# Kernel tuning notes

Hardware: AMD Instinct MI355X
Metric: run time of the kernel (lower is better)

Reference implementation:

```python
import jax, jax.numpy as jnp
import numpy as np

BITS = 4
PACK = 32 // BITS  # 8 nibbles per int32
GROUPSIZE = 128
MASK = (1 << BITS) - 1


def dequantize(qweight, qzeros, scales):
    """GPTQ dequant: W[i,o] = scales[g[i],o] * (q[i,o] - (z[g[i],o] + 1))."""
    shifts = (jnp.arange(PACK, dtype=jnp.int32) * BITS)
    # qweight: [in/8, out] packed along input dim -> [in, out]
    wq = (qweight[:, None, :] >> shifts[None, :, None]) & MASK
    wq = wq.reshape(-1, qweight.shape[1])  # [in, out] int32 in [0,15]
    # qzeros: [G, out/8] packed along output dim -> [G, out]
    zq = ((qzeros[:, :, None] >> shifts[None, None, :]) & MASK) + 1
    zq = zq.reshape(qzeros.shape[0], -1)  # [G, out]
    g_idx = jnp.arange(wq.shape[0], dtype=jnp.int32) // GROUPSIZE  # [in]
    # fp16 dequant like the CUDA/Triton GPTQ kernels
    W = (wq - zq[g_idx]).astype(jnp.float16) * scales[g_idx]
    return W  # [in, out] fp16


def setup_inputs() -> dict:
    key = jax.random.key(0)
    kx, kw, kz, ks, kb = jax.random.split(key, 5)
    in_f, out_f, groups = 4096, 4096, 4096 // GROUPSIZE
    x = jax.random.normal(kx, (8192, in_f), dtype=jnp.float16)
    qweight = jax.random.randint(kw, (in_f // PACK, out_f), 0, 2147483647, dtype=jnp.int32)
    qzeros = jax.random.randint(kz, (groups, out_f // PACK), 0, 2147483647, dtype=jnp.int32)
    scales = (jax.random.uniform(ks, (groups, out_f), dtype=jnp.float32) * 0.01 + 0.001).astype(jnp.float16)
    bias = jax.random.normal(kb, (out_f,), dtype=jnp.float16)
    return {"x": x, "qweight": qweight, "qzeros": qzeros, "scales": scales, "bias": bias}


def reference(x, qweight, qzeros, scales, bias):
    W = dequantize(qweight, qzeros, scales)  # [in, out] fp16
    # accumulate in fp32, output fp16 (matches CaiGPTQLinearOp fp16 output)
    out = jnp.matmul(x, W, preferred_element_type=jnp.float32).astype(jnp.float16)
    out = out + bias
    return out
```

## Files before the change

kernel.cpp:

```cpp
#include <hip/hip_runtime.h>

typedef _Float16 half8 __attribute__((ext_vector_type(8)));
typedef _Float16 half2v __attribute__((ext_vector_type(2)));
typedef float floatx4 __attribute__((ext_vector_type(4)));

#define K_IN 4096
#define N_OUT 4096
#define NGROUPS 32
#define BM 128
#define BN 128

__device__ __forceinline__ unsigned int pkcvt(float lo, float hi) {
    return __builtin_bit_cast(unsigned int, __builtin_amdgcn_cvt_pkrtz(lo, hi));
}

__device__ __forceinline__ void gll16(const _Float16* g, _Float16* l) {
    __builtin_amdgcn_global_load_lds(
        (const __attribute__((address_space(1))) void*)g,
        (__attribute__((address_space(3))) void*)l, 16, 0, 0);
}

__global__ __launch_bounds__(256)
void cvt_x_f16(const float* __restrict__ x, _Float16* __restrict__ x16) {
    const size_t idx = ((size_t)blockIdx.x * 256 + threadIdx.x) * 8;
    const float4 a = *(const float4*)(x + idx);
    const float4 b = *(const float4*)(x + idx + 4);
    uint4 u;
    u.x = pkcvt(a.x, a.y);  u.y = pkcvt(a.z, a.w);
    u.z = pkcvt(b.x, b.y);  u.w = pkcvt(b.z, b.w);
    *(uint4*)(x16 + idx) = u;
}

__global__ __launch_bounds__(256)
void dequant_wt(const int* __restrict__ qweight,
                const int* __restrict__ qzeros,
                const float* __restrict__ scales,
                _Float16* __restrict__ wt)
{
    const int tid = threadIdx.x;
    const int col = blockIdx.x * 64 + (tid & 63);
    const int g   = blockIdx.y;
    const int i   = tid >> 6;

    const unsigned int zw = (unsigned int)qzeros[g * (N_OUT / 8) + (col >> 3)];
    const unsigned int z  = (zw >> ((col & 7) * 4)) & 0xFu;
    const unsigned int cb = 0x6400u + z + 1u;
    const half2v c2 = __builtin_bit_cast(half2v, cb | (cb << 16));
    const float  s  = scales[g * N_OUT + col];
    const half2v s2 = __builtin_bit_cast(half2v, pkcvt(s, s));

    const int kc0 = g * 16 + i * 4;
#pragma unroll
    for (int r = 0; r < 4; ++r) {
        const unsigned int q = (unsigned int)qweight[(size_t)(kc0 + r) * N_OUT + col];
        const unsigned int r0 = (q & 0x000F000Fu)         | 0x64006400u;
        const unsigned int r1 = ((q >> 4) & 0x000F000Fu)  | 0x64006400u;
        const unsigned int r2 = ((q >> 8) & 0x000F000Fu)  | 0x64006400u;
        const unsigned int r3 = ((q >> 12) & 0x000F000Fu) | 0x64006400u;
        unsigned int p0 = __builtin_bit_cast(unsigned int,
                          (half2v)((__builtin_bit_cast(half2v, r0) - c2) * s2));
        unsigned int p1 = __builtin_bit_cast(unsigned int,
                          (half2v)((__builtin_bit_cast(half2v, r1) - c2) * s2));
        unsigned int p2 = __builtin_bit_cast(unsigned int,
                          (half2v)((__builtin_bit_cast(half2v, r2) - c2) * s2));
        unsigned int p3 = __builtin_bit_cast(unsigned int,
                          (half2v)((__builtin_bit_cast(half2v, r3) - c2) * s2));
        uint4 nat;
        nat.x = (p0 & 0xFFFFu) | (p1 << 16);
        nat.y = (p2 & 0xFFFFu) | (p3 << 16);
        nat.z = (p0 >> 16) | (p1 & 0xFFFF0000u);
        nat.w = (p2 >> 16) | (p3 & 0xFFFF0000u);
        *(uint4*)(wt + (size_t)col * K_IN + (kc0 + r) * 8) = nat;
    }
}

__global__ __launch_bounds__(256, 3)
void gemm_f16(const _Float16* __restrict__ x16,
              const _Float16* __restrict__ wt,
              const float* __restrict__ bias,
              float* __restrict__ out)
{
    __shared__ alignas(16) _Float16 As[2 * BM * 32];

    const int tid  = threadIdx.x;
    const int lane = tid & 63;
    const int wave = tid >> 6;
    const int l15  = lane & 15;
    const int l4   = lane >> 4;

    const int blockN = blockIdx.x * BN;
    const int blockM = blockIdx.y * BM;

    floatx4 acc[8][2] = {};

    const int grow  = wave * 32 + (lane >> 2);
    const int gchnk = (lane & 3) ^ ((lane >> 3) & 3);
    const _Float16* gsrc0 = x16 + (size_t)(blockM + grow) * K_IN + gchnk * 8;
    const _Float16* gsrc1 = gsrc0 + (size_t)16 * K_IN;
    _Float16* ldst0 = &As[wave * 1024];
    _Float16* ldst1 = ldst0 + 512;

    const int rdoff = (l4 ^ ((l15 >> 1) & 3)) * 8;

    int ncol[2];
    const _Float16* wp0;
    const _Float16* wp1;
    ncol[0] = blockN + wave * 32 + l15;
    ncol[1] = ncol[0] + 16;
    wp0 = wt + (size_t)ncol[0] * K_IN + l4 * 8;
    wp1 = wt + (size_t)ncol[1] * K_IN + l4 * 8;

    gll16(gsrc0, ldst0);
    gll16(gsrc1, ldst1);
    __builtin_amdgcn_sched_barrier(0);
    uint4 pw0 = *(const uint4*)(const void*)wp0;
    uint4 pw1 = *(const uint4*)(const void*)wp1;

    for (int t = 0; t < 4 * NGROUPS; ++t) {
        const int buf = t & 1;

        asm volatile("s_waitcnt vmcnt(2)" ::: "memory");
        __builtin_amdgcn_s_barrier();
        asm volatile("" ::: "memory");

        half8 afrag[8];
#pragma unroll
        for (int i = 0; i < 8; ++i)
            afrag[i] = *(const half8*)(const void*)
                &As[buf * 4096 + (i * 16 + l15) * 32 + rdoff];

        half8 b0 = __builtin_bit_cast(half8, pw0);
        half8 b1 = __builtin_bit_cast(half8, pw1);

        const int t1 = (t + 1 < 4 * NGROUPS) ? t + 1 : t;
        const int bn = buf ^ 1;
        gll16(gsrc0 + t1 * 32, ldst0 + bn * 4096);
        gll16(gsrc1 + t1 * 32, ldst1 + bn * 4096);
        __builtin_amdgcn_sched_barrier(0);
        pw0 = *(const uint4*)(const void*)(wp0 + t1 * 32);
        pw1 = *(const uint4*)(const void*)(wp1 + t1 * 32);

#pragma unroll
        for (int i = 0; i < 8; ++i) {
            acc[i][0] = __builtin_amdgcn_mfma_f32_16x16x32_f16(
                afrag[i], b0, acc[i][0], 0, 0, 0);
            acc[i][1] = __builtin_amdgcn_mfma_f32_16x16x32_f16(
                afrag[i], b1, acc[i][1], 0, 0, 0);
        }
    }

#pragma unroll
    for (int j = 0; j < 2; ++j) {
        const int n = ncol[j];
        const float bv = bias[n];
#pragma unroll
        for (int i = 0; i < 8; ++i) {
            const int m = blockM + i * 16 + l4 * 4;
#pragma unroll
            for (int r = 0; r < 4; ++r)
                out[(size_t)(m + r) * N_OUT + n] = acc[i][j][r] + bv;
        }
    }
}

__global__ __launch_bounds__(256, 2)
void gptq_gemm_fused(const float* __restrict__ x,
                     const int*   __restrict__ qweight,
                     const int*   __restrict__ qzeros,
                     const float* __restrict__ scales,
                     const float* __restrict__ bias,
                     float*       __restrict__ out)
{
#define LDA 40
    __shared__ alignas(16) _Float16 Asf[2][BM * LDA];

    const int tid  = threadIdx.x;
    const int lane = tid & 63;
    const int wave = tid >> 6;
    const int l15  = lane & 15;
    const int l4   = lane >> 4;

    const int blockN = blockIdx.x * BN;
    const int blockM = blockIdx.y * BM;

    floatx4 acc[8][2] = {};

    const int srow = tid >> 2;
    const int sch  = tid & 3;
    const float* xr0 = x + (size_t)(blockM + srow) * K_IN + sch * 8;
    const float* xr1 = xr0 + (size_t)64 * K_IN;
    _Float16* lw0 = &Asf[0][srow * LDA + sch * 8];
    _Float16* lw1 = &Asf[0][(srow + 64) * LDA + sch * 8];

    int ncol[2];
#pragma unroll
    for (int j = 0; j < 2; ++j) ncol[j] = blockN + wave * 32 + j * 16 + l15;

    unsigned int zraw[2]; float sraw[2];
#pragma unroll
    for (int j = 0; j < 2; ++j) {
        zraw[j] = (unsigned int)qzeros[ncol[j] >> 3];
        sraw[j] = scales[ncol[j]];
    }
    float4 pa0 = *(const float4*)(xr0);
    float4 pa1 = *(const float4*)(xr0 + 4);
    float4 pb0 = *(const float4*)(xr1);
    float4 pb1 = *(const float4*)(xr1 + 4);
    unsigned int pq[2];
    {
        const int* qr = qweight + (size_t)l4 * N_OUT;
#pragma unroll
        for (int j = 0; j < 2; ++j) pq[j] = (unsigned int)qr[ncol[j]];
    }

    for (int g = 0; g < NGROUPS; ++g) {
        unsigned int c2u[2], s2u[2];
#pragma unroll
        for (int j = 0; j < 2; ++j) {
            const unsigned int z  = (zraw[j] >> ((ncol[j] & 7) * 4)) & 0xFu;
            const unsigned int cb = 0x6400u + z + 1u;
            c2u[j] = cb | (cb << 16);
            s2u[j] = pkcvt(sraw[j], sraw[j]);
        }
        const int gn = (g + 1 < NGROUPS) ? g + 1 : g;
#pragma unroll
        for (int j = 0; j < 2; ++j) {
            zraw[j] = (unsigned int)qzeros[gn * (N_OUT / 8) + (ncol[j] >> 3)];
            sraw[j] = scales[gn * N_OUT + ncol[j]];
        }

#pragma unroll
        for (int kk = 0; kk < 4; ++kk) {
            const int t   = g * 4 + kk;
            const int buf = t & 1;

            uint4 ra, rb;
            ra.x = pkcvt(pa0.x, pa1.x);  ra.y = pkcvt(pa0.y, pa1.y);
            ra.z = pkcvt(pa0.z, pa1.z);  ra.w = pkcvt(pa0.w, pa1.w);
            rb.x = pkcvt(pb0.x, pb1.x);  rb.y = pkcvt(pb0.y, pb1.y);
            rb.z = pkcvt(pb0.z, pb1.z);  rb.w = pkcvt(pb0.w, pb1.w);
            *(uint4*)(void*)(lw0 + buf * (BM * LDA)) = ra;
            *(uint4*)(void*)(lw1 + buf * (BM * LDA)) = rb;

            unsigned int bq[2] = {pq[0], pq[1]};

            const int t1 = (t + 1 < 4 * NGROUPS) ? t + 1 : t;
            pa0 = *(const float4*)(xr0 + t1 * 32);
            pa1 = *(const float4*)(xr0 + t1 * 32 + 4);
            pb0 = *(const float4*)(xr1 + t1 * 32);
            pb1 = *(const float4*)(xr1 + t1 * 32 + 4);
            {
                const int* qr = qweight + (size_t)(t1 * 4 + l4) * N_OUT;
#pragma unroll
                for (int j = 0; j < 2; ++j) pq[j] = (unsigned int)qr[ncol[j]];
            }

            __syncthreads();

            half8 bfrag[2];
#pragma unroll
            for (int j = 0; j < 2; ++j) {
                const unsigned int q = bq[j];
                const unsigned int r0 = (q & 0x000F000Fu)        | 0x64006400u;
                const unsigned int r1 = ((q >> 4) & 0x000F000Fu) | 0x64006400u;
                const unsigned int r2 = ((q >> 8) & 0x000F000Fu) | 0x64006400u;
                const unsigned int r3 = ((q >> 12) & 0x000F000Fu)| 0x64006400u;
                const half2v c2 = __builtin_bit_cast(half2v, c2u[j]);
                const half2v s2 = __builtin_bit_cast(half2v, s2u[j]);
                union { unsigned int u[4]; half8 h; } pk;
                pk.u[0] = __builtin_bit_cast(unsigned int,
                          (half2v)((__builtin_bit_cast(half2v, r0) - c2) * s2));
                pk.u[1] = __builtin_bit_cast(unsigned int,
                          (half2v)((__builtin_bit_cast(half2v, r1) - c2) * s2));
                pk.u[2] = __builtin_bit_cast(unsigned int,
                          (half2v)((__builtin_bit_cast(half2v, r2) - c2) * s2));
                pk.u[3] = __builtin_bit_cast(unsigned int,
                          (half2v)((__builtin_bit_cast(half2v, r3) - c2) * s2));
                bfrag[j] = pk.h;
            }

            half8 afrag[8];
#pragma unroll
            for (int i = 0; i < 8; ++i)
                afrag[i] = *(const half8*)(const void*)
                    &Asf[buf][(i * 16 + l15) * LDA + l4 * 8];

#pragma unroll
            for (int i = 0; i < 8; ++i)
#pragma unroll
                for (int j = 0; j < 2; ++j)
                    acc[i][j] = __builtin_amdgcn_mfma_f32_16x16x32_f16(
                        afrag[i], bfrag[j], acc[i][j], 0, 0, 0);
        }
    }

#pragma unroll
    for (int j = 0; j < 2; ++j) {
        const int n = ncol[j];
        const float bv = bias[n];
#pragma unroll
        for (int i = 0; i < 8; ++i) {
            const int m = blockM + i * 16 + l4 * 4;
#pragma unroll
            for (int r = 0; r < 4; ++r)
                out[(size_t)(m + r) * N_OUT + n] = acc[i][j][r] + bv;
        }
    }
#undef LDA
}

extern "C" void kernel_launch(void* const* d_in, const int* in_sizes, int n_in,
                              void* d_out, int out_size, void* d_ws, size_t ws_size,
                              hipStream_t stream) {
    const float* x    = (const float*)d_in[0];
    const int*   qw   = (const int*)d_in[1];
    const int*   qz   = (const int*)d_in[2];
    const float* sc   = (const float*)d_in[3];
    const float* bias = (const float*)d_in[4];
    float*       out  = (float*)d_out;

    const int M = in_sizes[0] / K_IN;

    const size_t x16_bytes = (size_t)M * K_IN * sizeof(_Float16);
    const size_t wt_bytes  = (size_t)N_OUT * K_IN * sizeof(_Float16);

    if (ws_size >= x16_bytes + wt_bytes) {
        _Float16* x16 = (_Float16*)d_ws;
        _Float16* wtp = (_Float16*)((char*)d_ws + x16_bytes);

        cvt_x_f16<<<(int)((size_t)M * K_IN / 2048), 256, 0, stream>>>(x, x16);
        dequant_wt<<<dim3(N_OUT / 64, NGROUPS), 256, 0, stream>>>(qw, qz, sc, wtp);
        gemm_f16<<<dim3(N_OUT / BN, M / BM), 256, 0, stream>>>(x16, wtp, bias, out);
    } else {
        gptq_gemm_fused<<<dim3(N_OUT / BN, M / BM), 256, 0, stream>>>(
            x, qw, qz, sc, bias, out);
    }
}
```

Before: 560.3 us.

## Replace GEMM with 256x256 tile, 8-wave, LDS-staged A/B phased pipeline

Replaces the 128x128 GEMM, which streamed B fragments directly from global memory, with a 512-thread kernel computing 256x256 tiles. Both A and B are staged into XOR-swizzled LDS via global_load_lds with a two-stage buffer, and each K-step is split into four compute phases that interleave staging loads with MFMAs under raised wave priority. It also remaps workgroup IDs so that consecutive blocks are spread across N and M tiles for better L2 locality. This cuts global traffic per FLOP, at the cost of more LDS use, more barriers and higher register pressure, and it now requires M to be a multiple of 256.

```diff
diff --git a/kernel.cpp b/kernel.cpp
--- a/kernel.cpp
+++ b/kernel.cpp
@@ -7,8 +7,6 @@
 #define K_IN 4096
 #define N_OUT 4096
 #define NGROUPS 32
-#define BM 128
-#define BN 128
 
 __device__ __forceinline__ unsigned int pkcvt(float lo, float hi) {
     return __builtin_bit_cast(unsigned int, __builtin_amdgcn_cvt_pkrtz(lo, hi));
@@ -74,95 +72,138 @@
     }
 }
 
-__global__ __launch_bounds__(256, 3)
-void gemm_f16(const _Float16* __restrict__ x16,
-              const _Float16* __restrict__ wt,
-              const float* __restrict__ bias,
-              float* __restrict__ out)
+
+#define BARRIER() asm volatile("s_barrier" ::: "memory")
+#define VMCNT2()  asm volatile("s_waitcnt vmcnt(2)" ::: "memory")
+
+#define STAGE_A(d, half, kt)                                                   \
+    do {                                                                       \
+        gll16(aS + (size_t)((half) * 128) * K_IN + (kt) * 64,                  \
+              ashW + (d) * 16384 + (half) * 8192);                             \
+        gll16(aS + (size_t)((half) * 128 + 64) * K_IN + (kt) * 64,             \
+              ashW + (d) * 16384 + (half) * 8192 + 4096);                      \
+    } while (0)
+#define STAGE_B(d, half, kt)                                                   \
+    do {                                                                       \
+        gll16(bS + (size_t)((half) * 128) * K_IN + (kt) * 64,                  \
+              bshW + (d) * 16384 + (half) * 8192);                             \
+        gll16(bS + (size_t)((half) * 128 + 64) * K_IN + (kt) * 64,             \
+              bshW + (d) * 16384 + (half) * 8192 + 4096);                      \
+    } while (0)
+
+#define PH_BODY(d, q, STAGE_STMT, MID_BARRIER)                                 \
+    {                                                                          \
+        const int dbase = (d) * 16384;                                         \
+        half8 af[4][2]; half8 bf[2][2];                                        \
+        _Pragma("unroll")                                                      \
+        for (int m = 0; m < 4; ++m) {                                          \
+            const int ro = dbase + aRow + (((q) & 1) * 4 + m) * 1024;          \
+            af[m][0] = *(const half8*)(const void*)&Ash[ro + c0];              \
+            af[m][1] = *(const half8*)(const void*)&Ash[ro + (c0 ^ 32)];       \
+        }                                                                      \
+        _Pragma("unroll")                                                      \
+        for (int n = 0; n < 2; ++n) {                                          \
+            const int ro = dbase + bRow + (((q) >> 1) * 2 + n) * 1024;         \
+            bf[n][0] = *(const half8*)(const void*)&Bsh[ro + c0];              \
+            bf[n][1] = *(const half8*)(const void*)&Bsh[ro + (c0 ^ 32)];       \
+        }                                                                      \
+        STAGE_STMT;                                                            \
+        MID_BARRIER;                                                           \
+        __builtin_amdgcn_s_setprio(1);                                         \
+        _Pragma("unroll")                                                      \
+        for (int m = 0; m < 4; ++m)                                            \
+            _Pragma("unroll")                                                  \
+            for (int n = 0; n < 2; ++n) {                                      \
+                acc[((q) & 1) * 4 + m][((q) >> 1) * 2 + n] =                   \
+                    __builtin_amdgcn_mfma_f32_16x16x32_f16(                    \
+                        af[m][0], bf[n][0],                                    \
+                        acc[((q) & 1) * 4 + m][((q) >> 1) * 2 + n], 0, 0, 0);  \
+                acc[((q) & 1) * 4 + m][((q) >> 1) * 2 + n] =                   \
+                    __builtin_amdgcn_mfma_f32_16x16x32_f16(                    \
+                        af[m][1], bf[n][1],                                    \
+                        acc[((q) & 1) * 4 + m][((q) >> 1) * 2 + n], 0, 0, 0);  \
+            }                                                                  \
+        __builtin_amdgcn_s_setprio(0);                                         \
+        BARRIER();                                                             \
+    }
+
+__global__ __launch_bounds__(512, 2)
+void gemm_f16_8ph(const _Float16* __restrict__ x16,
+                  const _Float16* __restrict__ wt,
+                  const float* __restrict__ bias,
+                  float* __restrict__ out)
 {
-    __shared__ alignas(16) _Float16 As[2 * BM * 32];
+    __shared__ alignas(16) _Float16 Ash[2 * 256 * 64];
+    __shared__ alignas(16) _Float16 Bsh[2 * 256 * 64];
 
     const int tid  = threadIdx.x;
     const int lane = tid & 63;
     const int wave = tid >> 6;
+    const int wm   = wave >> 2;
+    const int wn   = wave & 3;
     const int l15  = lane & 15;
     const int l4   = lane >> 4;
 
-    const int blockN = blockIdx.x * BN;
-    const int blockM = blockIdx.y * BM;
-
-    floatx4 acc[8][2] = {};
-
-    const int grow  = wave * 32 + (lane >> 2);
-    const int gchnk = (lane & 3) ^ ((lane >> 3) & 3);
-    const _Float16* gsrc0 = x16 + (size_t)(blockM + grow) * K_IN + gchnk * 8;
-    const _Float16* gsrc1 = gsrc0 + (size_t)16 * K_IN;
-    _Float16* ldst0 = &As[wave * 1024];
-    _Float16* ldst1 = ldst0 + 512;
-
-    const int rdoff = (l4 ^ ((l15 >> 1) & 3)) * 8;
-
-    int ncol[2];
-    const _Float16* wp0;
-    const _Float16* wp1;
-    ncol[0] = blockN + wave * 32 + l15;
-    ncol[1] = ncol[0] + 16;
-    wp0 = wt + (size_t)ncol[0] * K_IN + l4 * 8;
-    wp1 = wt + (size_t)ncol[1] * K_IN + l4 * 8;
-
-    gll16(gsrc0, ldst0);
-    gll16(gsrc1, ldst1);
-    __builtin_amdgcn_sched_barrier(0);
-    uint4 pw0 = *(const uint4*)(const void*)wp0;
-    uint4 pw1 = *(const uint4*)(const void*)wp1;
-
-    for (int t = 0; t < 4 * NGROUPS; ++t) {
-        const int buf = t & 1;
-
-        asm volatile("s_waitcnt vmcnt(2)" ::: "memory");
-        __builtin_amdgcn_s_barrier();
-        asm volatile("" ::: "memory");
-
-        half8 afrag[8];
-#pragma unroll
-        for (int i = 0; i < 8; ++i)
-            afrag[i] = *(const half8*)(const void*)
-                &As[buf * 4096 + (i * 16 + l15) * 32 + rdoff];
-
-        half8 b0 = __builtin_bit_cast(half8, pw0);
-        half8 b1 = __builtin_bit_cast(half8, pw1);
-
-        const int t1 = (t + 1 < 4 * NGROUPS) ? t + 1 : t;
-        const int bn = buf ^ 1;
-        gll16(gsrc0 + t1 * 32, ldst0 + bn * 4096);
-        gll16(gsrc1 + t1 * 32, ldst1 + bn * 4096);
-        __builtin_amdgcn_sched_barrier(0);
-        pw0 = *(const uint4*)(const void*)(wp0 + t1 * 32);
-        pw1 = *(const uint4*)(const void*)(wp1 + t1 * 32);
-
-#pragma unroll
-        for (int i = 0; i < 8; ++i) {
-            acc[i][0] = __builtin_amdgcn_mfma_f32_16x16x32_f16(
-                afrag[i], b0, acc[i][0], 0, 0, 0);
-            acc[i][1] = __builtin_amdgcn_mfma_f32_16x16x32_f16(
-                afrag[i], b1, acc[i][1], 0, 0, 0);
-        }
-    }
-
-#pragma unroll
-    for (int j = 0; j < 2; ++j) {
-        const int n = ncol[j];
-        const float bv = bias[n];
-#pragma unroll
-        for (int i = 0; i < 8; ++i) {
-            const int m = blockM + i * 16 + l4 * 4;
+    const int nwg = gridDim.x;
+    const int lin = blockIdx.x;
+    const int wg  = (lin & 7) * (nwg >> 3) + (lin >> 3);
+    const int blockN = (wg & 15) * 256;
+    const int blockM = (wg >> 4) * 256;
+
+    floatx4 acc[8][4] = {};
+
+    const int srow = tid >> 3;
+    const int lchk = (tid & 7) ^ ((tid >> 3) & 7);
+    const _Float16* aS = x16 + (size_t)(blockM + srow) * K_IN + lchk * 8;
+    const _Float16* bS = wt  + (size_t)(blockN + srow) * K_IN + lchk * 8;
+    _Float16* ashW = &Ash[wave * 512];
+    _Float16* bshW = &Bsh[wave * 512];
+
+    const int aRow = (wm * 128 + l15) * 64;
+    const int bRow = (wn * 64 + l15) * 64;
+    const int c0   = (l4 ^ (l15 & 7)) * 8;
+
+    STAGE_A(0, 0, 0);
+    STAGE_A(0, 1, 0);
+    STAGE_B(0, 0, 0);
+    STAGE_B(0, 1, 0);
+
+    for (int i = 0; i < 32; ++i) {
+        const int kt1 = 2 * i + 1;
+        const int kt2 = (2 * i + 2 < 64) ? 2 * i + 2 : 63;
+
+        STAGE_A(1, 0, kt1);
+        VMCNT2();
+        BARRIER();
+        PH_BODY(0, 0, (void)0, (void)0)
+        PH_BODY(0, 1, STAGE_A(1, 1, kt1), BARRIER())
+        PH_BODY(0, 2, STAGE_B(1, 0, kt1), BARRIER())
+        PH_BODY(0, 3, STAGE_B(1, 1, kt1), BARRIER())
+        STAGE_A(0, 0, kt2);
+        VMCNT2();
+        BARRIER();
+        PH_BODY(1, 0, (void)0, (void)0)
+        PH_BODY(1, 1, STAGE_A(0, 1, kt2), BARRIER())
+        PH_BODY(1, 2, STAGE_B(0, 0, kt2), BARRIER())
+        PH_BODY(1, 3, STAGE_B(0, 1, kt2), BARRIER())
+    }
+
+#pragma unroll
+    for (int n = 0; n < 4; ++n) {
+        const int col = blockN + wn * 64 + n * 16 + l15;
+        const float bv = bias[col];
+#pragma unroll
+        for (int m = 0; m < 8; ++m) {
+            const int row = blockM + wm * 128 + m * 16 + l4 * 4;
 #pragma unroll
             for (int r = 0; r < 4; ++r)
-                out[(size_t)(m + r) * N_OUT + n] = acc[i][j][r] + bv;
-        }
-    }
-}
-
+                out[(size_t)(row + r) * N_OUT + col] = acc[m][n][r] + bv;
+        }
+    }
+}
+
+#define BM 128
+#define BN 128
 __global__ __launch_bounds__(256, 2)
 void gptq_gemm_fused(const float* __restrict__ x,
                      const int*   __restrict__ qweight,
@@ -324,13 +365,14 @@
     const size_t x16_bytes = (size_t)M * K_IN * sizeof(_Float16);
     const size_t wt_bytes  = (size_t)N_OUT * K_IN * sizeof(_Float16);
 
-    if (ws_size >= x16_bytes + wt_bytes) {
+    if (ws_size >= x16_bytes + wt_bytes && (M % 256) == 0) {
         _Float16* x16 = (_Float16*)d_ws;
         _Float16* wtp = (_Float16*)((char*)d_ws + x16_bytes);
 
         cvt_x_f16<<<(int)((size_t)M * K_IN / 2048), 256, 0, stream>>>(x, x16);
         dequant_wt<<<dim3(N_OUT / 64, NGROUPS), 256, 0, stream>>>(qw, qz, sc, wtp);
-        gemm_f16<<<dim3(N_OUT / BN, M / BM), 256, 0, stream>>>(x16, wtp, bias, out);
+        const int nwg = (M / 256) * (N_OUT / 256);
+        gemm_f16_8ph<<<nwg, 512, 0, stream>>>(x16, wtp, bias, out);
     } else {
         gptq_gemm_fused<<<dim3(N_OUT / BN, M / BM), 256, 0, stream>>>(
             x, qw, qz, sc, bias, out);
```

Measured after the change: 592.2 us. +5.7%, slower.
